# Optimization experiments

Measured on AMD Instinct MI355X. Metric: run time of the kernel, lower is better.

The kernel has to match this reference:

```python
import jax, jax.numpy as jnp
import numpy as np

DIM_X = 100   # equation.dim_x
DIM_Y = 1     # equation.dim_y
DIM_D = 100   # equation.dim_d
DIM_H = 512   # dim_h
T_END = 1.0   # equation.T
BN_EPS = 1e-5
SQRT2 = float(np.sqrt(2.0))


def _linear_init(k, fan_in, fan_out):
    lim = 1.0 / np.sqrt(fan_in)
    kw, kb = jax.random.split(k)
    W = jax.random.uniform(kw, (fan_in, fan_out), minval=-lim, maxval=lim, dtype=jnp.float32)
    b = jax.random.uniform(kb, (fan_out,), minval=-lim, maxval=lim, dtype=jnp.float32)
    return W, b


def setup_inputs() -> dict:
    key = jax.random.key(0)
    ks = jax.random.split(key, 6)
    W1, b1 = _linear_init(ks[0], DIM_X + 1, DIM_H)
    W2, b2 = _linear_init(ks[1], DIM_H, DIM_H)
    W3, b3 = _linear_init(ks[2], DIM_H, DIM_H)
    W4, b4 = _linear_init(ks[3], DIM_H, DIM_Y * DIM_D)
    # y_0 = guess_y_0[0]*l + guess_y_0[1]*(1-l), l~U(0,1); guesses (0,1) -> y_0~U(0,1)
    y_0 = jax.random.uniform(ks[4], (DIM_Y,), dtype=jnp.float32)
    x_0 = jnp.zeros((DIM_X,), dtype=jnp.float32)  # equation.x_0
    g1 = jnp.ones((DIM_H,), jnp.float32); be1 = jnp.zeros((DIM_H,), jnp.float32)
    g2 = jnp.ones((DIM_H,), jnp.float32); be2 = jnp.zeros((DIM_H,), jnp.float32)
    return dict(y_0=y_0, W1=W1, b1=b1, W2=W2, b2=b2, W3=W3, b3=b3, W4=W4, b4=b4,
                g1=g1, be1=be1, g2=g2, be2=be2, x_0=x_0, batch_size=4096, N=64)


def reference(y_0, W1, b1, W2, b2, W3, b3, W4, b4, g1, be1, g2, be2, x_0, batch_size, N):
    dt = T_END / N
    sqrt_dt = float(np.sqrt(dt))

    def bn(h, g, be):  # training-mode BatchNorm1d: biased batch stats
        m = jnp.mean(h, axis=0)
        v = jnp.mean(jnp.square(h - m), axis=0)
        return g * (h - m) * jax.lax.rsqrt(v + BN_EPS) + be

    def get_z(x, t):
        h = jnp.concatenate([x, jnp.full((x.shape[0], 1), t, x.dtype)], axis=1)
        h = jax.nn.gelu(h @ W1 + b1, approximate=False)
        h = bn(jax.nn.gelu(h @ W2 + b2, approximate=False), g1, be1)
        h = bn(jax.nn.gelu(h @ W3 + b3, approximate=False), g2, be2)
        return (h @ W4 + b4).reshape(-1, DIM_Y, DIM_D)  # [B, dy, dd]

    x = jnp.broadcast_to(x_0, (batch_size, DIM_X))
    y = jnp.broadcast_to(y_0, (batch_size, DIM_Y))
    ts = jnp.arange(N, dtype=jnp.float32) * dt
    keys = jax.random.split(jax.random.key(42), N)

    def step(carry, inp):
        x, y = carry
        t, k = inp
        z = get_z(x, t)
        dW = jax.random.normal(k, (x.shape[0], DIM_D), dtype=x.dtype) * sqrt_dt
        # b(t,x,y)=0, sigma(t,x)=sqrt(2)*I  =>  x += sqrt(2)*dW
        x = x + SQRT2 * dW
        # f(t,x,y,z) = -0.5*||z||^2 (per dim_y row); z@dW contraction over dim_d
        f = -0.5 * jnp.sum(z * z, axis=2)                 # [B, dy]
        y = y - f * dt + jnp.einsum('byd,bd->by', z, dW)  # [B, dy]
        return (x, y), None

    (x, y), _ = jax.lax.scan(step, (x, y), (ts, keys))
    return x, y
```

## Files before the change

kernel.cpp:

```cpp
#include <hip/hip_runtime.h>
#include <hip/hip_bf16.h>
#include <stdint.h>

#define B 4096
#define DX 100
#define H 512
#define DD 100
#define NSTEPS 64
#define KIN 128
#define N4 128
#define NBLK 256
#define NTHR 512

typedef short bf8 __attribute__((ext_vector_type(8)));
typedef float f32x4 __attribute__((ext_vector_type(4)));

__device__ __forceinline__ ushort f2bf(float f) {
  union { __hip_bfloat16 h; ushort u; } cv;
  cv.h = __float2bfloat16(f);
  return cv.u;
}
__device__ __forceinline__ float bf2f(ushort h) {
  return __uint_as_float((uint32_t)h << 16);
}
__device__ __forceinline__ f32x4 mfma16(bf8 a, bf8 b, f32x4 c) {
  return __builtin_amdgcn_mfma_f32_16x16x32_bf16(a, b, c, 0, 0, 0);
}

__device__ __forceinline__ int aload_i(int* p) {
  return __hip_atomic_load(p, __ATOMIC_RELAXED, __HIP_MEMORY_SCOPE_AGENT);
}
__device__ __forceinline__ float aload_f(const float* p) {
  return __hip_atomic_load((float*)p, __ATOMIC_RELAXED, __HIP_MEMORY_SCOPE_AGENT);
}

__device__ __forceinline__ void tf2x32(uint32_t k0, uint32_t k1,
                                       uint32_t x0, uint32_t x1,
                                       uint32_t& o0, uint32_t& o1)
{
  uint32_t ks2 = 0x1BD11BDAu ^ k0 ^ k1;
  x0 += k0; x1 += k1;
#define RND(r) { x0 += x1; x1 = (x1 << (r)) | (x1 >> (32 - (r))); x1 ^= x0; }
  RND(13) RND(15) RND(26) RND(6)   x0 += k1;  x1 += ks2 + 1u;
  RND(17) RND(29) RND(16) RND(24)  x0 += ks2; x1 += k0  + 2u;
  RND(13) RND(15) RND(26) RND(6)   x0 += k0;  x1 += k1  + 3u;
  RND(17) RND(29) RND(16) RND(24)  x0 += k1;  x1 += ks2 + 4u;
  RND(13) RND(15) RND(26) RND(6)   x0 += ks2; x1 += k0  + 5u;
#undef RND
  o0 = x0; o1 = x1;
}
__device__ __forceinline__ void step_keys(int step, uint32_t& k0, uint32_t& k1)
{
  tf2x32(0u, 42u, 0u, (uint32_t)step, k0, k1);
}
__device__ __forceinline__ uint32_t jax_bits(uint32_t k0, uint32_t k1, uint32_t m)
{
  uint32_t a, b;
  tf2x32(k0, k1, 0u, m, a, b);
  return a ^ b;
}

__device__ __forceinline__ float jax_normal_from_bits(uint32_t bits)
{
  float f = __uint_as_float((bits >> 9) | 0x3f800000u) - 1.0f;
  const float lo = -0.99999994f;
  float u = fmaxf(lo, f * 2.0f + lo);
  float w = -log1pf(-u * u);
  float p;
  if (w < 5.0f) {
    w -= 2.5f;
    p =          2.81022636e-08f;
    p = fmaf(p, w, 3.43273939e-07f);
    p = fmaf(p, w, -3.5233877e-06f);
    p = fmaf(p, w, -4.39150654e-06f);
    p = fmaf(p, w, 0.00021858087f);
    p = fmaf(p, w, -0.00125372503f);
    p = fmaf(p, w, -0.00417768164f);
    p = fmaf(p, w, 0.246640727f);
    p = fmaf(p, w, 1.50140941f);
  } else {
    w = sqrtf(w) - 3.0f;
    p =          -0.000200214257f;
    p = fmaf(p, w, 0.000100950558f);
    p = fmaf(p, w, 0.00134934322f);
    p = fmaf(p, w, -0.00367342844f);
    p = fmaf(p, w, 0.00573950773f);
    p = fmaf(p, w, -0.0076224613f);
    p = fmaf(p, w, 0.00943887047f);
    p = fmaf(p, w, 1.00167406f);
    p = fmaf(p, w, 2.83297682f);
  }
  return 1.4142135623730951f * (p * u);
}

__device__ __forceinline__ float gelu(float v)
{
  float v2 = v * v;
  float zin = fmaf(0.044715f * v2, v, v);
  float z = fminf(1.5957691216057308f * zin, 80.0f);
  float e = __expf(z);
  float t = (e - 1.0f) * __builtin_amdgcn_rcpf(e + 1.0f);
  float hv = 0.5f * v;
  return fmaf(hv, t, hv);
}

__global__ void k_prep(const float* __restrict__ W1, const float* __restrict__ W2,
                       const float* __restrict__ W3, const float* __restrict__ W4,
                       ushort* __restrict__ w1t, ushort* __restrict__ w2t,
                       ushort* __restrict__ w3t, ushort* __restrict__ w4t)
{
  int gid = blockIdx.x * blockDim.x + threadIdx.x;
  int stride = gridDim.x * blockDim.x;
  for (int i = gid; i < H * KIN; i += stride) {
    int c = i >> 7, k = i & (KIN - 1);
    w1t[i] = f2bf(k < 101 ? W1[k * H + c] : 0.0f);
  }
  for (int i = gid; i < H * H; i += stride) {
    int c = i >> 9, k = i & (H - 1);
    w2t[i] = f2bf(W2[k * H + c]);
    w3t[i] = f2bf(W3[k * H + c]);
  }
  for (int i = gid; i < N4 * H; i += stride) {
    int c = i >> 9, k = i & (H - 1);
    w4t[i] = f2bf(c < DD ? W4[k * DD + c] : 0.0f);
  }
}


__global__ void k_init_chunk(const float* __restrict__ y0, const float* __restrict__ x0,
                             float* __restrict__ x_run, float* __restrict__ y,
                             float* __restrict__ bn)
{
  int gid = blockIdx.x * blockDim.x + threadIdx.x;
  int stride = gridDim.x * blockDim.x;
  for (int i = gid; i < B * DX; i += stride) x_run[i] = x0[i % DX];
  for (int i = gid; i < B; i += stride) y[i] = y0[0];
  for (int i = gid; i < NSTEPS * 4 * H; i += stride) bn[i] = 0.0f;
}

__global__ void k_xs(float* __restrict__ x_run, ushort* __restrict__ xs,
                     float* __restrict__ xout, int s0, int Sc)
{
  int gid = blockIdx.x * blockDim.x + threadIdx.x;
  int row = gid >> 7, col = gid & 127;
  const float dt = 1.0f / NSTEPS;
  if (col < DX) {
    float xr = x_run[row * DX + col];
    uint32_t m = (uint32_t)(row * DD + col);
    for (int t = 0; t < Sc; ++t) {
      xs[t * (B * KIN) + row * KIN + col] = f2bf(xr);
      uint32_t k0, k1;
      step_keys(s0 + t, k0, k1);
      float dW = 0.125f * jax_normal_from_bits(jax_bits(k0, k1, m));
      xr += 1.4142135623730951f * dW;
    }
    x_run[row * DX + col] = xr;
    if (s0 + Sc == NSTEPS) xout[row * DX + col] = xr;
  } else {
    for (int t = 0; t < Sc; ++t)
      xs[t * (B * KIN) + row * KIN + col] =
          (col == DX) ? f2bf((float)(s0 + t) * dt) : (ushort)0;
  }
}

__global__ __launch_bounds__(512, 4) void kL12(
    const ushort* __restrict__ xs, const ushort* __restrict__ w1t,
    const float* __restrict__ b1, const ushort* __restrict__ w2t,
    const float* __restrict__ b2, ushort* __restrict__ gb,
    float* __restrict__ bn, int s0)
{
  __shared__ ushort xt[64][136];
  __shared__ ushort at[64][264];
  const int tid = threadIdx.x;
  const int mb = blockIdx.x;
  const int base = mb * 64;
  float* bns = bn + (s0 + (mb >> 6)) * 4 * H;
  float* bnq = bns + H;
  const int w = tid >> 6, lane = tid & 63, lr = lane & 15, lg = lane >> 4;

  for (int i = tid; i < 64 * 16; i += 512) {
    int r = i >> 4, kk = (i & 15) * 8;
    *(bf8*)&xt[r][kk] = *(const bf8*)&xs[(base + r) * KIN + kk];
  }

  f32x4 acc[4][4];
#pragma unroll
  for (int mi = 0; mi < 4; mi++)
#pragma unroll
    for (int t = 0; t < 4; t++) acc[mi][t] = (f32x4)(0.0f);

#pragma unroll
  for (int c = 0; c < 2; c++) {
    __syncthreads();
#pragma unroll
    for (int u = 0; u < 2; u++) {
      f32x4 a1[4];
#pragma unroll
      for (int mi = 0; mi < 4; mi++) a1[mi] = (f32x4)(0.0f);
#pragma unroll
      for (int ks = 0; ks < 4; ks++) {
        int hcol = c * 256 + w * 32 + u * 16 + lr;
        bf8 b = *(const bf8*)(w1t + hcol * KIN + ks * 32 + lg * 8);
#pragma unroll
        for (int mi = 0; mi < 4; mi++) {
          bf8 a = *(const bf8*)&xt[mi * 16 + lr][ks * 32 + lg * 8];
          a1[mi] = mfma16(a, b, a1[mi]);
        }
      }
      int lcol = w * 32 + u * 16 + lr;
      float bb = b1[c * 256 + lcol];
#pragma unroll
      for (int mi = 0; mi < 4; mi++)
#pragma unroll
        for (int r = 0; r < 4; r++)
          at[mi * 16 + lg * 4 + r][lcol] = f2bf(gelu(a1[mi][r] + bb));
    }
    __syncthreads();
#pragma unroll
    for (int ks = 0; ks < 8; ks++) {
      bf8 af[4];
#pragma unroll
      for (int mi = 0; mi < 4; mi++)
        af[mi] = *(const bf8*)&at[mi * 16 + lr][ks * 32 + lg * 8];
#pragma unroll
      for (int t = 0; t < 4; t++) {
        int col = w * 64 + t * 16 + lr;
        bf8 b = *(const bf8*)(w2t + col * H + c * 256 + ks * 32 + lg * 8);
#pragma unroll
        for (int mi = 0; mi < 4; mi++) acc[mi][t] = mfma16(af[mi], b, acc[mi][t]);
      }
    }
  }

#pragma unroll
  for (int t = 0; t < 4; t++) {
    int col = w * 64 + t * 16 + lr;
    float bb = b2[col], s = 0.0f, q = 0.0f;
#pragma unroll
    for (int mi = 0; mi < 4; mi++)
#pragma unroll
      for (int r = 0; r < 4; r++) {
        float v = gelu(acc[mi][t][r] + bb);
        gb[(base + mi * 16 + lg * 4 + r) * H + col] = f2bf(v);
        s += v; q += v * v;
      }
    s += __shfl_xor(s, 16); s += __shfl_xor(s, 32);
    q += __shfl_xor(q, 16); q += __shfl_xor(q, 32);
    if (lane < 16) { unsafeAtomicAdd(&bns[col], s); unsafeAtomicAdd(&bnq[col], q); }
  }
}

__global__ __launch_bounds__(512, 4) void kL3(
    const ushort* __restrict__ gb, float* __restrict__ bn, int s0,
    const float* __restrict__ gamma, const float* __restrict__ beta,
    const ushort* __restrict__ w3t, const float* __restrict__ b3,
    ushort* __restrict__ ga)
{
  __shared__ float sc[H], sh[H];
  __shared__ ushort at[64][264];
  const int tid = threadIdx.x;
  const int mb = blockIdx.x;
  const int base = mb * 64;
  float* bn1s = bn + (s0 + (mb >> 6)) * 4 * H;
  float* bn1q = bn1s + H;
  float* bn2s = bn1s + 2 * H;
  float* bn2q = bn1s + 3 * H;
  const int w = tid >> 6, lane = tid & 63, lr = lane & 15, lg = lane >> 4;

  for (int c = tid; c < H; c += 512) {
    float m = bn1s[c] * (1.0f / B);
    float v = bn1q[c] * (1.0f / B) - m * m;
    float s2_ = gamma[c] * rsqrtf(v + 1e-5f);
    sc[c] = s2_; sh[c] = beta[c] - m * s2_;
  }

  f32x4 acc[4][4];
#pragma unroll
  for (int mi = 0; mi < 4; mi++)
#pragma unroll
    for (int t = 0; t < 4; t++) acc[mi][t] = (f32x4)(0.0f);

#pragma unroll
  for (int c = 0; c < 2; c++) {
    __syncthreads();
    for (int i = tid; i < 4096; i += 512) {
      int r = i >> 6, k4 = (i & 63) * 4, gk = c * 256 + k4;
      ushort4 gv = *(const ushort4*)&gb[(base + r) * H + gk];
      ushort4 o;
      o.x = f2bf(fmaf(bf2f(gv.x), sc[gk + 0], sh[gk + 0]));
      o.y = f2bf(fmaf(bf2f(gv.y), sc[gk + 1], sh[gk + 1]));
      o.z = f2bf(fmaf(bf2f(gv.z), sc[gk + 2], sh[gk + 2]));
      o.w = f2bf(fmaf(bf2f(gv.w), sc[gk + 3], sh[gk + 3]));
      *(ushort4*)&at[r][k4] = o;
    }
    __syncthreads();
#pragma unroll
    for (int ks = 0; ks < 8; ks++) {
      bf8 af[4];
#pragma unroll
      for (int mi = 0; mi < 4; mi++)
        af[mi] = *(const bf8*)&at[mi * 16 + lr][ks * 32 + lg * 8];
#pragma unroll
      for (int t = 0; t < 4; t++) {
        int col = w * 64 + t * 16 + lr;
        bf8 b = *(const bf8*)(w3t + col * H + c * 256 + ks * 32 + lg * 8);
#pragma unroll
        for (int mi = 0; mi < 4; mi++) acc[mi][t] = mfma16(af[mi], b, acc[mi][t]);
      }
    }
  }

#pragma unroll
  for (int t = 0; t < 4; t++) {
    int col = w * 64 + t * 16 + lr;
    float bb = b3[col], s = 0.0f, q = 0.0f;
#pragma unroll
    for (int mi = 0; mi < 4; mi++)
#pragma unroll
      for (int r = 0; r < 4; r++) {
        float v = gelu(acc[mi][t][r] + bb);
        ga[(base + mi * 16 + lg * 4 + r) * H + col] = f2bf(v);
        s += v; q += v * v;
      }
    s += __shfl_xor(s, 16); s += __shfl_xor(s, 32);
    q += __shfl_xor(q, 16); q += __shfl_xor(q, 32);
    if (lane < 16) { unsafeAtomicAdd(&bn2s[col], s); unsafeAtomicAdd(&bn2q[col], q); }
  }
}

__global__ __launch_bounds__(512, 2) void kL4(
    const ushort* __restrict__ ga, const float* __restrict__ bn, int s0,
    const float* __restrict__ gamma, const float* __restrict__ beta,
    const ushort* __restrict__ w4t, const float* __restrict__ b4,
    float* __restrict__ y)
{
  __shared__ float sc[H], sh[H];
  __shared__ ushort at[32 * 520];
  __shared__ float ys1[8][32], ys2[8][32];
  const int tid = threadIdx.x;
  const int sb = blockIdx.x >> 7;
  const int s = s0 + sb;
  const int lb = (blockIdx.x & 127) * 32;
  const int rbase = sb * B + lb;
  const float dt = 1.0f / NSTEPS;
  const float* bn2s = bn + s * 4 * H + 2 * H;
  const float* bn2q = bn2s + H;

  for (int c = tid; c < H; c += 512) {
    float m = bn2s[c] * (1.0f / B);
    float v = bn2q[c] * (1.0f / B) - m * m;
    float s2_ = gamma[c] * rsqrtf(v + 1e-5f);
    sc[c] = s2_; sh[c] = beta[c] - m * s2_;
  }
  __syncthreads();
  for (int i = tid; i < 32 * 128; i += 512) {
    int r = i >> 7, k4 = (i & 127) * 4;
    ushort4 gv = *(const ushort4*)&ga[(rbase + r) * H + k4];
    ushort4 o;
    o.x = f2bf(fmaf(bf2f(gv.x), sc[k4 + 0], sh[k4 + 0]));
    o.y = f2bf(fmaf(bf2f(gv.y), sc[k4 + 1], sh[k4 + 1]));
    o.z = f2bf(fmaf(bf2f(gv.z), sc[k4 + 2], sh[k4 + 2]));
    o.w = f2bf(fmaf(bf2f(gv.w), sc[k4 + 3], sh[k4 + 3]));
    *(ushort4*)&at[r * 520 + k4] = o;
  }
  __syncthreads();

  const int w = tid >> 6, lane = tid & 63, lr = lane & 15, lg = lane >> 4;
  const int col = w * 16 + lr;
  f32x4 acc[2];
  acc[0] = (f32x4)(0.0f); acc[1] = (f32x4)(0.0f);
#pragma unroll
  for (int ks = 0; ks < 16; ks++) {
    bf8 b = *(const bf8*)(w4t + col * H + ks * 32 + lg * 8);
#pragma unroll
    for (int mi = 0; mi < 2; mi++) {
      bf8 a = *(const bf8*)&at[(mi * 16 + lr) * 520 + ks * 32 + lg * 8];
      acc[mi] = mfma16(a, b, acc[mi]);
    }
  }

  uint32_t k0, k1;
  step_keys(s, k0, k1);
#pragma unroll
  for (int mi = 0; mi < 2; mi++) {
    float zz[4] = {0, 0, 0, 0}, zw[4] = {0, 0, 0, 0};
    if (col < DD) {
      float bb = b4[col];
#pragma unroll
      for (int r = 0; r < 4; r++) {
        int lrow = lb + mi * 16 + lg * 4 + r;
        float z = acc[mi][r] + bb;
        uint32_t m = (uint32_t)lrow * (uint32_t)DD + (uint32_t)col;
        float dW = 0.125f * jax_normal_from_bits(jax_bits(k0, k1, m));
        zz[r] = z * z;
        zw[r] = z * dW;
      }
    }
#pragma unroll
    for (int r = 0; r < 4; r++) {
      zz[r] += __shfl_xor(zz[r], 1); zz[r] += __shfl_xor(zz[r], 2);
      zz[r] += __shfl_xor(zz[r], 4); zz[r] += __shfl_xor(zz[r], 8);
      zw[r] += __shfl_xor(zw[r], 1); zw[r] += __shfl_xor(zw[r], 2);
      zw[r] += __shfl_xor(zw[r], 4); zw[r] += __shfl_xor(zw[r], 8);
    }
    if (lr == 0) {
#pragma unroll
      for (int r = 0; r < 4; r++) {
        ys1[w][mi * 16 + lg * 4 + r] = zz[r];
        ys2[w][mi * 16 + lg * 4 + r] = zw[r];
      }
    }
  }
  __syncthreads();
  if (tid < 32) {
    float s1 = 0.0f, s2_ = 0.0f;
#pragma unroll
    for (int i = 0; i < 8; i++) { s1 += ys1[i][tid]; s2_ += ys2[i][tid]; }
    unsafeAtomicAdd(&y[lb + tid], 0.5f * dt * s1 + s2_);
  }
}


__device__ __forceinline__ void gbar(int* cnt, int* gen, int mode)
{
  if (mode) __builtin_amdgcn_fence(__ATOMIC_RELEASE, "agent");
  __syncthreads();
  if (threadIdx.x == 0) {
    int g = aload_i(gen);
    int a = __hip_atomic_fetch_add(cnt, 1, __ATOMIC_RELAXED, __HIP_MEMORY_SCOPE_AGENT);
    if (a == NBLK - 1) {
      __hip_atomic_store(cnt, 0, __ATOMIC_RELAXED, __HIP_MEMORY_SCOPE_AGENT);
      __hip_atomic_store(gen, g + 1, __ATOMIC_RELAXED, __HIP_MEMORY_SCOPE_AGENT);
    } else {
      while (aload_i(gen) == g) __builtin_amdgcn_s_sleep(2);
    }
  }
  __syncthreads();
  if (mode) __builtin_amdgcn_fence(__ATOMIC_ACQUIRE, "agent");
  else      asm volatile("buffer_inv" ::: "memory");
}

__global__ void k_init_coop(const float* __restrict__ y0, const float* __restrict__ x0,
                            float* __restrict__ x, float* __restrict__ y,
                            float* __restrict__ bn, int* __restrict__ bar)
{
  int gid = blockIdx.x * blockDim.x + threadIdx.x;
  int stride = gridDim.x * blockDim.x;
  for (int i = gid; i < B * DX; i += stride) x[i] = x0[i % DX];
  for (int i = gid; i < B; i += stride) y[i] = y0[0];
  for (int i = gid; i < NSTEPS * 4 * H; i += stride) bn[i] = 0.0f;
  if (gid < 32) bar[gid] = 0;
}

__device__ __forceinline__ void l1_sec(const ushort* xt, const ushort* __restrict__ w1t,
                                       const float* __restrict__ b1,
                                       ushort* __restrict__ h1g,
                                       int base, int w, int lr, int lg)
{
  f32x4 a1[4];
#pragma unroll
  for (int t = 0; t < 4; t++) a1[t] = (f32x4)(0.0f);
#pragma unroll
  for (int ks = 0; ks < 4; ks++) {
    bf8 a = *(const bf8*)&xt[lr * 136 + ks * 32 + lg * 8];
#pragma unroll
    for (int t = 0; t < 4; t++) {
      int cc = w * 64 + t * 16 + lr;
      bf8 bfr = *(const bf8*)(w1t + cc * KIN + ks * 32 + lg * 8);
      a1[t] = mfma16(a, bfr, a1[t]);
    }
  }
#pragma unroll
  for (int t = 0; t < 4; t++) {
    int cc = w * 64 + t * 16 + lr;
    float bb = b1[cc];
#pragma unroll
    for (int r = 0; r < 4; r++)
      h1g[(base + lg * 4 + r) * H + cc] = f2bf(gelu(a1[t][r] + bb));
  }
}

__global__ void __launch_bounds__(NTHR, 2) k_steps(
    const ushort* __restrict__ w1t, const float* __restrict__ b1,
    const ushort* __restrict__ w2t, const float* __restrict__ b2,
    const ushort* __restrict__ w3t, const float* __restrict__ b3,
    const ushort* __restrict__ w4t, const float* __restrict__ b4,
    const float* __restrict__ ga1, const float* __restrict__ be1,
    const float* __restrict__ ga2, const float* __restrict__ be2,
    ushort* __restrict__ g1, ushort* __restrict__ g2h,
    float* __restrict__ bn, float* __restrict__ x, float* __restrict__ y,
    int* __restrict__ bar)
{
  __shared__ ushort smem[64 * 264];
  __shared__ float sc[H], sh[H];
  __shared__ float ys1[8][16], ys2[8][16];
  __shared__ int dsh[2];

  const int tid = threadIdx.x;
  const int w = tid >> 6, lane = tid & 63, lr = lane & 15, lg = lane >> 4;
  const float dt = 1.0f / NSTEPS;
  int* cnt = bar; int* gen = bar + 1;
  int* bins = bar + 2;
  int* gcnt = bar + 18;

  int sgs, mode;
  {
    if (tid == 0) {
      uint32_t xcc = __builtin_amdgcn_s_getreg(20 | (31 << 11)) & 15u;
      int j = __hip_atomic_fetch_add(&bins[xcc], 1, __ATOMIC_RELAXED, __HIP_MEMORY_SCOPE_AGENT);
      dsh[0] = (int)xcc; dsh[1] = j;
    }
    gbar(cnt, gen, 1);
    if (tid == 0) {
      int ok = 1;
      for (int k = 0; k < 8; k++)  ok &= (aload_i(&bins[k]) == 32);
      for (int k = 8; k < 16; k++) ok &= (aload_i(&bins[k]) == 0);
      if (ok) { dsh[0] = dsh[0] * 32 + dsh[1]; dsh[1] = 0; }
      else {
        dsh[0] = __hip_atomic_fetch_add(gcnt, 1, __ATOMIC_RELAXED, __HIP_MEMORY_SCOPE_AGENT);
        dsh[1] = 1;
      }
    }
    __syncthreads();
    sgs = dsh[0]; mode = dsh[1];
  }
  const int mb = sgs >> 2, q = sgs & 3;
  const int cbase = sgs * 16;

  {
    ushort* xt = smem;
    for (int i = tid; i < 16 * KIN; i += NTHR) {
      int r = i >> 7, k = i & (KIN - 1);
      xt[r * 136 + k] = (k < DX) ? f2bf(x[(cbase + r) * DX + k]) : (ushort)0;
    }
    __syncthreads();
    l1_sec(xt, w1t, b1, g2h, cbase, w, lr, lg);
  }
  gbar(cnt, gen, mode);

  for (int s = 0; s < NSTEPS; ++s) {
    float* bn1s = bn + s * 4 * H;
    float* bn1q = bn1s + H;
    float* bn2s = bn1s + 2 * H;
    float* bn2q = bn1s + 3 * H;

    {
      const int col = q * 128 + w * 16 + lr;
      f32x4 acc[4];
#pragma unroll
      for (int mi = 0; mi < 4; mi++) acc[mi] = (f32x4)(0.0f);
#pragma unroll
      for (int c = 0; c < 2; c++) {
        if (c) __syncthreads();
        for (int i = tid; i < 2048; i += NTHR) {
          int r = i >> 5, kk = (i & 31) * 8;
          *(bf8*)&smem[r * 264 + kk] = *(const bf8*)&g2h[(mb * 64 + r) * H + c * 256 + kk];
        }
        __syncthreads();
#pragma unroll
        for (int ks = 0; ks < 8; ks++) {
          bf8 b = *(const bf8*)(w2t + col * H + c * 256 + ks * 32 + lg * 8);
#pragma unroll
          for (int mi = 0; mi < 4; mi++) {
            bf8 a = *(const bf8*)&smem[(mi * 16 + lr) * 264 + ks * 32 + lg * 8];
            acc[mi] = mfma16(a, b, acc[mi]);
          }
        }
      }
      float bb = b2[col], ssum = 0.0f, qsum = 0.0f;
#pragma unroll
      for (int mi = 0; mi < 4; mi++)
#pragma unroll
        for (int r = 0; r < 4; r++) {
          float v = gelu(acc[mi][r] + bb);
          g1[(mb * 64 + mi * 16 + lg * 4 + r) * H + col] = f2bf(v);
          ssum += v; qsum += v * v;
        }
      ssum += __shfl_xor(ssum, 16); ssum += __shfl_xor(ssum, 32);
      qsum += __shfl_xor(qsum, 16); qsum += __shfl_xor(qsum, 32);
      if (lane < 16) { unsafeAtomicAdd(&bn1s[col], ssum); unsafeAtomicAdd(&bn1q[col], qsum); }
    }
    gbar(cnt, gen, mode);

    {
      const int col = q * 128 + w * 16 + lr;
      for (int c = tid; c < H; c += NTHR) {
        float m = aload_f(&bn1s[c]) * (1.0f / B);
        float v = aload_f(&bn1q[c]) * (1.0f / B) - m * m;
        float s2_ = ga1[c] * rsqrtf(v + 1e-5f);
        sc[c] = s2_; sh[c] = be1[c] - m * s2_;
      }
      __syncthreads();
      f32x4 acc[4];
#pragma unroll
      for (int mi = 0; mi < 4; mi++) acc[mi] = (f32x4)(0.0f);
#pragma unroll
      for (int c = 0; c < 2; c++) {
        if (c) __syncthreads();
        for (int i = tid; i < 4096; i += NTHR) {
          int r = i >> 6, k4 = (i & 63) * 4, gk = c * 256 + k4;
          ushort4 gv = *(const ushort4*)&g1[(mb * 64 + r) * H + gk];
          ushort4 o;
          o.x = f2bf(fmaf(bf2f(gv.x), sc[gk + 0], sh[gk + 0]));
          o.y = f2bf(fmaf(bf2f(gv.y), sc[gk + 1], sh[gk + 1]));
          o.z = f2bf(fmaf(bf2f(gv.z), sc[gk + 2], sh[gk + 2]));
          o.w = f2bf(fmaf(bf2f(gv.w), sc[gk + 3], sh[gk + 3]));
          *(ushort4*)&smem[r * 264 + k4] = o;
        }
        __syncthreads();
#pragma unroll
        for (int ks = 0; ks < 8; ks++) {
          bf8 b = *(const bf8*)(w3t + col * H + c * 256 + ks * 32 + lg * 8);
#pragma unroll
          for (int mi = 0; mi < 4; mi++) {
            bf8 a = *(const bf8*)&smem[(mi * 16 + lr) * 264 + ks * 32 + lg * 8];
            acc[mi] = mfma16(a, b, acc[mi]);
          }
        }
      }
      float bb = b3[col], ssum = 0.0f, qsum = 0.0f;
#pragma unroll
      for (int mi = 0; mi < 4; mi++)
#pragma unroll
        for (int r = 0; r < 4; r++) {
          float v = gelu(acc[mi][r] + bb);
          g2h[(mb * 64 + mi * 16 + lg * 4 + r) * H + col] = f2bf(v);
          ssum += v; qsum += v * v;
        }
      ssum += __shfl_xor(ssum, 16); ssum += __shfl_xor(ssum, 32);
      qsum += __shfl_xor(qsum, 16); qsum += __shfl_xor(qsum, 32);
      if (lane < 16) { unsafeAtomicAdd(&bn2s[col], ssum); unsafeAtomicAdd(&bn2q[col], qsum); }
    }
    gbar(cnt, gen, mode);

    {
      ushort* at16 = smem;
      ushort* xt   = smem + 16 * 520;
      for (int c = tid; c < H; c += NTHR) {
        float m = aload_f(&bn2s[c]) * (1.0f / B);
        float v = aload_f(&bn2q[c]) * (1.0f / B) - m * m;
        float s2_ = ga2[c] * rsqrtf(v + 1e-5f);
        sc[c] = s2_; sh[c] = be2[c] - m * s2_;
      }
      __syncthreads();
      for (int i = tid; i < 2048; i += NTHR) {
        int r = i >> 7, k4 = (i & 127) * 4;
        ushort4 gv = *(const ushort4*)&g2h[(cbase + r) * H + k4];
        ushort4 o;
        o.x = f2bf(fmaf(bf2f(gv.x), sc[k4 + 0], sh[k4 + 0]));
        o.y = f2bf(fmaf(bf2f(gv.y), sc[k4 + 1], sh[k4 + 1]));
        o.z = f2bf(fmaf(bf2f(gv.z), sc[k4 + 2], sh[k4 + 2]));
        o.w = f2bf(fmaf(bf2f(gv.w), sc[k4 + 3], sh[k4 + 3]));
        *(ushort4*)&at16[r * 520 + k4] = o;
      }
      __syncthreads();

      const int col = w * 16 + lr;
      f32x4 acc = (f32x4)(0.0f);
#pragma unroll
      for (int ks = 0; ks < 16; ks++) {
        bf8 a = *(const bf8*)&at16[lr * 520 + ks * 32 + lg * 8];
        bf8 b = *(const bf8*)(w4t + col * H + ks * 32 + lg * 8);
        acc = mfma16(a, b, acc);
      }

      uint32_t k0, k1;
      step_keys(s, k0, k1);
      float zz[4] = {0, 0, 0, 0}, zw[4] = {0, 0, 0, 0};
      float tnext = (float)(s + 1) * dt;
      if (col < DD) {
        float bb = b4[col];
#pragma unroll
        for (int r = 0; r < 4; r++) {
          int row = lg * 4 + r, grow = cbase + row;
          float z = acc[r] + bb;
          uint32_t m = (uint32_t)grow * (uint32_t)DD + (uint32_t)col;
          float dW = 0.125f * jax_normal_from_bits(jax_bits(k0, k1, m));
          float xn = x[grow * DX + col] + 1.4142135623730951f * dW;
          x[grow * DX + col] = xn;
          xt[row * 136 + col] = f2bf(xn);
          zz[r] = z * z;
          zw[r] = z * dW;
        }
      } else {
#pragma unroll
        for (int r = 0; r < 4; r++)
          xt[(lg * 4 + r) * 136 + col] = (col == DX) ? f2bf(tnext) : (ushort)0;
      }
#pragma unroll
      for (int r = 0; r < 4; r++) {
        zz[r] += __shfl_xor(zz[r], 1); zz[r] += __shfl_xor(zz[r], 2);
        zz[r] += __shfl_xor(zz[r], 4); zz[r] += __shfl_xor(zz[r], 8);
        zw[r] += __shfl_xor(zw[r], 1); zw[r] += __shfl_xor(zw[r], 2);
        zw[r] += __shfl_xor(zw[r], 4); zw[r] += __shfl_xor(zw[r], 8);
      }
      if (lr == 0) {
#pragma unroll
        for (int r = 0; r < 4; r++) {
          ys1[w][lg * 4 + r] = zz[r];
          ys2[w][lg * 4 + r] = zw[r];
        }
      }
      __syncthreads();
      if (tid < 16) {
        float s1 = 0.0f, s2_ = 0.0f;
#pragma unroll
        for (int i = 0; i < 8; i++) { s1 += ys1[i][tid]; s2_ += ys2[i][tid]; }
        y[cbase + tid] += 0.5f * dt * s1 + s2_;
      }
      if (s < NSTEPS - 1)
        l1_sec(xt, w1t, b1, g2h, cbase, w, lr, lg);
    }
    if (s < NSTEPS - 1) gbar(cnt, gen, mode);
  }
}


extern "C" void kernel_launch(void* const* d_in, const int* in_sizes, int n_in,
                              void* d_out, int out_size, void* d_ws, size_t ws_size,
                              hipStream_t stream)
{
  const float* y0  = (const float*)d_in[0];
  const float* W1  = (const float*)d_in[1];
  const float* b1  = (const float*)d_in[2];
  const float* W2  = (const float*)d_in[3];
  const float* b2  = (const float*)d_in[4];
  const float* W3  = (const float*)d_in[5];
  const float* b3  = (const float*)d_in[6];
  const float* W4  = (const float*)d_in[7];
  const float* b4  = (const float*)d_in[8];
  const float* ga1 = (const float*)d_in[9];
  const float* be1 = (const float*)d_in[10];
  const float* ga2 = (const float*)d_in[11];
  const float* be2 = (const float*)d_in[12];
  const float* x0  = (const float*)d_in[13];

  float* x = (float*)d_out;
  float* y = x + B * DX;

  const size_t fixed_b = (size_t)NSTEPS * 4 * H * 4 + (size_t)B * DX * 4 +
                         (size_t)(H * KIN + H * H + H * H + N4 * H) * 2;
  const size_t per_b = (size_t)B * H * 2 * 2;
  long smax = ((long)ws_size - (long)fixed_b) / (long)per_b;
  int S = (int)(smax < 64 ? smax : 64);

  if (S >= 1) {
    float* bn    = (float*)d_ws;
    float* x_run = bn + NSTEPS * 4 * H;
    ushort* w1t = (ushort*)(x_run + B * DX);
    ushort* w2t = w1t + H * KIN;
    ushort* w3t = w2t + H * H;
    ushort* w4t = w3t + H * H;
    ushort* ga  = w4t + N4 * H;
    ushort* gb  = ga + (size_t)S * B * H;
    ushort* xs  = ga;

    k_init_chunk<<<256, 256, 0, stream>>>(y0, x0, x_run, y, bn);
    k_prep<<<512, 256, 0, stream>>>(W1, W2, W3, W4, w1t, w2t, w3t, w4t);

    for (int s0 = 0; s0 < NSTEPS; s0 += S) {
      int Sc = (NSTEPS - s0 < S) ? (NSTEPS - s0) : S;
      k_xs<<<(B * KIN) / 256, 256, 0, stream>>>(x_run, xs, x, s0, Sc);
      kL12<<<Sc * 64, 512, 0, stream>>>(xs, w1t, b1, w2t, b2, gb, bn, s0);
      kL3 <<<Sc * 64, 512, 0, stream>>>(gb, bn, s0, ga1, be1, w3t, b3, ga);
      kL4 <<<Sc * 128, 512, 0, stream>>>(ga, bn, s0, ga2, be2, w4t, b4, y);
    }
  } else {
    int*   bar = (int*)d_ws;
    float* bn  = (float*)d_ws + 32;
    ushort* ub  = (ushort*)(bn + NSTEPS * 4 * H);
    ushort* g1  = ub;
    ushort* g2h = g1 + B * H;
    ushort* w1t = g2h + B * H;
    ushort* w2t = w1t + H * KIN;
    ushort* w3t = w2t + H * H;
    ushort* w4t = w3t + H * H;

    k_init_coop<<<256, 256, 0, stream>>>(y0, x0, x, y, bn, bar);
    k_prep<<<512, 256, 0, stream>>>(W1, W2, W3, W4, w1t, w2t, w3t, w4t);

    void* args[] = {
      (void*)&w1t, (void*)&b1, (void*)&w2t, (void*)&b2,
      (void*)&w3t, (void*)&b3, (void*)&w4t, (void*)&b4,
      (void*)&ga1, (void*)&be1, (void*)&ga2, (void*)&be2,
      (void*)&g1, (void*)&g2h, (void*)&bn, (void*)&x, (void*)&y, (void*)&bar
    };
    hipLaunchCooperativeKernel((const void*)k_steps, dim3(NBLK), dim3(NTHR),
                               args, 0, stream);
  }
}
```

Measured before the change: 1.411 ms.

## Stage GEMM epilogues through LDS for coalesced stores and share one activation buffer

The kL12 and kL3 epilogues now write GELU outputs into the shared-memory tile first, then store them to global memory as 16-byte coalesced rows instead of scattered 2-byte stores. kL3 overwrites its input activation buffer in place, so a single activation buffer replaces the separate ga and gb buffers, with xs given its own region. The workspace per step shrinks, which can allow larger step chunks. kL12 also drops the LDS copy of the input x tile and reads the A fragments straight from global memory. In exchange the epilogue gains extra barriers, and in-place overwrite in kL3 relies on each block reading its rows fully before writing them.

Measured after the change: 1.569 ms. 1.11x slower.

```diff
diff --git a/kernel.cpp b/kernel.cpp
--- a/kernel.cpp
+++ b/kernel.cpp
@@ -166,10 +166,9 @@
 __global__ __launch_bounds__(512, 4) void kL12(
     const ushort* __restrict__ xs, const ushort* __restrict__ w1t,
     const float* __restrict__ b1, const ushort* __restrict__ w2t,
-    const float* __restrict__ b2, ushort* __restrict__ gb,
+    const float* __restrict__ b2, ushort* __restrict__ g,
     float* __restrict__ bn, int s0)
 {
-  __shared__ ushort xt[64][136];
   __shared__ ushort at[64][264];
   const int tid = threadIdx.x;
   const int mb = blockIdx.x;
@@ -178,11 +177,6 @@
   float* bnq = bns + H;
   const int w = tid >> 6, lane = tid & 63, lr = lane & 15, lg = lane >> 4;
 
-  for (int i = tid; i < 64 * 16; i += 512) {
-    int r = i >> 4, kk = (i & 15) * 8;
-    *(bf8*)&xt[r][kk] = *(const bf8*)&xs[(base + r) * KIN + kk];
-  }
-
   f32x4 acc[4][4];
 #pragma unroll
   for (int mi = 0; mi < 4; mi++)
@@ -191,7 +185,7 @@
 
 #pragma unroll
   for (int c = 0; c < 2; c++) {
-    __syncthreads();
+    if (c) __syncthreads();
 #pragma unroll
     for (int u = 0; u < 2; u++) {
       f32x4 a1[4];
@@ -203,7 +197,7 @@
         bf8 b = *(const bf8*)(w1t + hcol * KIN + ks * 32 + lg * 8);
 #pragma unroll
         for (int mi = 0; mi < 4; mi++) {
-          bf8 a = *(const bf8*)&xt[mi * 16 + lr][ks * 32 + lg * 8];
+          bf8 a = *(const bf8*)(xs + (size_t)(base + mi * 16 + lr) * KIN + ks * 32 + lg * 8);
           a1[mi] = mfma16(a, b, a1[mi]);
         }
       }
@@ -233,28 +227,40 @@
   }
 
 #pragma unroll
-  for (int t = 0; t < 4; t++) {
-    int col = w * 64 + t * 16 + lr;
-    float bb = b2[col], s = 0.0f, q = 0.0f;
-#pragma unroll
-    for (int mi = 0; mi < 4; mi++)
-#pragma unroll
-      for (int r = 0; r < 4; r++) {
-        float v = gelu(acc[mi][t][r] + bb);
-        gb[(base + mi * 16 + lg * 4 + r) * H + col] = f2bf(v);
-        s += v; q += v * v;
-      }
-    s += __shfl_xor(s, 16); s += __shfl_xor(s, 32);
-    q += __shfl_xor(q, 16); q += __shfl_xor(q, 32);
-    if (lane < 16) { unsafeAtomicAdd(&bns[col], s); unsafeAtomicAdd(&bnq[col], q); }
+  for (int p = 0; p < 2; p++) {
+    __syncthreads();
+#pragma unroll
+    for (int tt = 0; tt < 2; tt++) {
+      int t = 2 * p + tt;
+      int col = w * 64 + t * 16 + lr;
+      float bb = b2[col], s = 0.0f, q = 0.0f;
+#pragma unroll
+      for (int mi = 0; mi < 4; mi++)
+#pragma unroll
+        for (int r = 0; r < 4; r++) {
+          float v = gelu(acc[mi][t][r] + bb);
+          at[mi * 16 + lg * 4 + r][w * 32 + tt * 16 + lr] = f2bf(v);
+          s += v; q += v * v;
+        }
+      s += __shfl_xor(s, 16); s += __shfl_xor(s, 32);
+      q += __shfl_xor(q, 16); q += __shfl_xor(q, 32);
+      if (lane < 16) { unsafeAtomicAdd(&bns[col], s); unsafeAtomicAdd(&bnq[col], q); }
+    }
+    __syncthreads();
+#pragma unroll
+    for (int k = 0; k < 4; k++) {
+      int slot = tid + k * 512;
+      int row = slot >> 5, jc = slot & 31;
+      int gcol = (jc >> 2) * 64 + 32 * p + (jc & 3) * 8;
+      *(bf8*)&g[(size_t)(base + row) * H + gcol] = *(const bf8*)&at[row][jc * 8];
+    }
   }
 }
 
 __global__ __launch_bounds__(512, 4) void kL3(
-    const ushort* __restrict__ gb, float* __restrict__ bn, int s0,
+    ushort* __restrict__ g, float* __restrict__ bn, int s0,
     const float* __restrict__ gamma, const float* __restrict__ beta,
-    const ushort* __restrict__ w3t, const float* __restrict__ b3,
-    ushort* __restrict__ ga)
+    const ushort* __restrict__ w3t, const float* __restrict__ b3)
 {
   __shared__ float sc[H], sh[H];
   __shared__ ushort at[64][264];
@@ -285,7 +291,7 @@
     __syncthreads();
     for (int i = tid; i < 4096; i += 512) {
       int r = i >> 6, k4 = (i & 63) * 4, gk = c * 256 + k4;
-      ushort4 gv = *(const ushort4*)&gb[(base + r) * H + gk];
+      ushort4 gv = *(const ushort4*)&g[(size_t)(base + r) * H + gk];
       ushort4 o;
       o.x = f2bf(fmaf(bf2f(gv.x), sc[gk + 0], sh[gk + 0]));
       o.y = f2bf(fmaf(bf2f(gv.y), sc[gk + 1], sh[gk + 1]));
@@ -311,25 +317,38 @@
   }
 
 #pragma unroll
-  for (int t = 0; t < 4; t++) {
-    int col = w * 64 + t * 16 + lr;
-    float bb = b3[col], s = 0.0f, q = 0.0f;
-#pragma unroll
-    for (int mi = 0; mi < 4; mi++)
-#pragma unroll
-      for (int r = 0; r < 4; r++) {
-        float v = gelu(acc[mi][t][r] + bb);
-        ga[(base + mi * 16 + lg * 4 + r) * H + col] = f2bf(v);
-        s += v; q += v * v;
-      }
-    s += __shfl_xor(s, 16); s += __shfl_xor(s, 32);
-    q += __shfl_xor(q, 16); q += __shfl_xor(q, 32);
-    if (lane < 16) { unsafeAtomicAdd(&bn2s[col], s); unsafeAtomicAdd(&bn2q[col], q); }
+  for (int p = 0; p < 2; p++) {
+    __syncthreads();
+#pragma unroll
+    for (int tt = 0; tt < 2; tt++) {
+      int t = 2 * p + tt;
+      int col = w * 64 + t * 16 + lr;
+      float bb = b3[col], s = 0.0f, q = 0.0f;
+#pragma unroll
+      for (int mi = 0; mi < 4; mi++)
+#pragma unroll
+        for (int r = 0; r < 4; r++) {
+          float v = gelu(acc[mi][t][r] + bb);
+          at[mi * 16 + lg * 4 + r][w * 32 + tt * 16 + lr] = f2bf(v);
+          s += v; q += v * v;
+        }
+      s += __shfl_xor(s, 16); s += __shfl_xor(s, 32);
+      q += __shfl_xor(q, 16); q += __shfl_xor(q, 32);
+      if (lane < 16) { unsafeAtomicAdd(&bn2s[col], s); unsafeAtomicAdd(&bn2q[col], q); }
+    }
+    __syncthreads();
+#pragma unroll
+    for (int k = 0; k < 4; k++) {
+      int slot = tid + k * 512;
+      int row = slot >> 5, jc = slot & 31;
+      int gcol = (jc >> 2) * 64 + 32 * p + (jc & 3) * 8;
+      *(bf8*)&g[(size_t)(base + row) * H + gcol] = *(const bf8*)&at[row][jc * 8];
+    }
   }
 }
 
 __global__ __launch_bounds__(512, 2) void kL4(
-    const ushort* __restrict__ ga, const float* __restrict__ bn, int s0,
+    const ushort* __restrict__ g, const float* __restrict__ bn, int s0,
     const float* __restrict__ gamma, const float* __restrict__ beta,
     const ushort* __restrict__ w4t, const float* __restrict__ b4,
     float* __restrict__ y)
@@ -355,7 +374,7 @@
   __syncthreads();
   for (int i = tid; i < 32 * 128; i += 512) {
     int r = i >> 7, k4 = (i & 127) * 4;
-    ushort4 gv = *(const ushort4*)&ga[(rbase + r) * H + k4];
+    ushort4 gv = *(const ushort4*)&g[(size_t)(rbase + r) * H + k4];
     ushort4 o;
     o.x = f2bf(fmaf(bf2f(gv.x), sc[k4 + 0], sh[k4 + 0]));
     o.y = f2bf(fmaf(bf2f(gv.y), sc[k4 + 1], sh[k4 + 1]));
@@ -740,7 +759,7 @@
 
   const size_t fixed_b = (size_t)NSTEPS * 4 * H * 4 + (size_t)B * DX * 4 +
                          (size_t)(H * KIN + H * H + H * H + N4 * H) * 2;
-  const size_t per_b = (size_t)B * H * 2 * 2;
+  const size_t per_b = (size_t)B * H * 2 + (size_t)B * KIN * 2;
   long smax = ((long)ws_size - (long)fixed_b) / (long)per_b;
   int S = (int)(smax < 64 ? smax : 64);
 
@@ -751,9 +770,8 @@
     ushort* w2t = w1t + H * KIN;
     ushort* w3t = w2t + H * H;
     ushort* w4t = w3t + H * H;
-    ushort* ga  = w4t + N4 * H;
-    ushort* gb  = ga + (size_t)S * B * H;
-    ushort* xs  = ga;
+    ushort* g   = w4t + N4 * H;
+    ushort* xs  = g + (size_t)S * B * H;
 
     k_init_chunk<<<256, 256, 0, stream>>>(y0, x0, x_run, y, bn);
     k_prep<<<512, 256, 0, stream>>>(W1, W2, W3, W4, w1t, w2t, w3t, w4t);
@@ -761,9 +779,9 @@
     for (int s0 = 0; s0 < NSTEPS; s0 += S) {
       int Sc = (NSTEPS - s0 < S) ? (NSTEPS - s0) : S;
       k_xs<<<(B * KIN) / 256, 256, 0, stream>>>(x_run, xs, x, s0, Sc);
-      kL12<<<Sc * 64, 512, 0, stream>>>(xs, w1t, b1, w2t, b2, gb, bn, s0);
-      kL3 <<<Sc * 64, 512, 0, stream>>>(gb, bn, s0, ga1, be1, w3t, b3, ga);
-      kL4 <<<Sc * 128, 512, 0, stream>>>(ga, bn, s0, ga2, be2, w4t, b4, y);
+      kL12<<<Sc * 64, 512, 0, stream>>>(xs, w1t, b1, w2t, b2, g, bn, s0);
+      kL3 <<<Sc * 64, 512, 0, stream>>>(g, bn, s0, ga1, be1, w3t, b3);
+      kL4 <<<Sc * 128, 512, 0, stream>>>(g, bn, s0, ga2, be2, w4t, b4, y);
     }
   } else {
     int*   bar = (int*)d_ws;
```
